# Kernel optimization log

Hardware: AMD Instinct MI355X
Metric: run time of the kernel (lower is better)

The kernel has to match this reference:

```python
import jax, jax.numpy as jnp
import numpy as np

ALPHA = 0.2  # LeakyReLU negative slope


def setup_inputs() -> dict:
    key = jax.random.key(0)
    k1, k2, k3 = jax.random.split(key, 3)
    B, N, F_in, F_out = 8, 2048, 256, 256
    h = jax.random.normal(k1, (B, N, F_in), dtype=jnp.float32)
    adj = jax.random.randint(k2, (B, N, N), 0, 2, dtype=jnp.int32)
    # xavier_uniform for W [F_in, F_out]
    limit = float(np.sqrt(6.0 / (F_in + F_out)))
    W = jax.random.uniform(k3, (F_in, F_out), dtype=jnp.float32, minval=-limit, maxval=limit)
    return {"h": h, "adj": adj, "W": W}


def reference(h, adj, W):
    # h: [B,N,F_in], W: [F_in,F_out] -> Wh: [B,N,F_out]
    Wh = jnp.einsum('bnf,fo->bno', h, W)
    # (Wh_i + Wh_j).sum(-1) == s[p] + s[q] with s = Wh.sum(-1); avoids [B,N,N,F] tensor
    s = Wh.sum(axis=-1)  # [B,N]
    e = jax.nn.leaky_relu(s[:, :, None] + s[:, None, :], negative_slope=ALPHA)  # [B,N,N]
    e = jnp.where(adj == 0, -jnp.inf, e)
    alpha = jax.nn.softmax(e, axis=-1)  # masked softmax over neighbors
    # dropout is identity in eval mode
    h_prime = jnp.einsum('bpq,bqo->bpo', alpha, Wh)  # [B,N,F_out]
    return h_prime
```

## Files before the change

### kernel.cpp

```cpp
#include <hip/hip_runtime.h>
#include <hip/hip_bf16.h>
#include <stdint.h>

#define LEAKY_ALPHA 0.2f

using f32x4 = __attribute__((ext_vector_type(4))) float;
using u32x2 = __attribute__((ext_vector_type(2))) unsigned int;
using u32x4 = __attribute__((ext_vector_type(4))) unsigned int;
using i32x4 = __attribute__((ext_vector_type(4))) int;
using s16x8 = __attribute__((ext_vector_type(8))) short;

static __device__ __forceinline__ unsigned short f2bf(float x) {
  __hip_bfloat16 b = __float2bfloat16(x);
  return __builtin_bit_cast(unsigned short, b);
}

__global__ __launch_bounds__(256) void gat_prep(
    const float* __restrict__ W, __hip_bfloat16* __restrict__ WT,
    float* __restrict__ wsum)
{
  const int o = blockIdx.x;
  const int t = threadIdx.x;
  WT[o * 256 + t] = __float2bfloat16(W[t * 256 + o]);
  float u = W[o * 256 + t];
#pragma unroll
  for (int off = 1; off < 64; off <<= 1) u += __shfl_xor(u, off, 64);
  __shared__ float red[4];
  if ((t & 63) == 0) red[t >> 6] = u;
  __syncthreads();
  if (t == 0) wsum[o] = red[0] + red[1] + red[2] + red[3];
}

__global__ __launch_bounds__(256) void gat_wh2(
    const float* __restrict__ h, const __hip_bfloat16* __restrict__ WT,
    const float* __restrict__ wsum, __hip_bfloat16* __restrict__ WhT,
    float* __restrict__ s)
{
  const int b = blockIdx.x >> 5;
  const int q0 = (blockIdx.x & 31) * 64;
  const int t = threadIdx.x;
  const int wid = t >> 6, lane = t & 63;

  __shared__ __align__(16) unsigned char Bh[64 * 512];
  __shared__ __align__(16) unsigned char Aw[256 * 128];
  __shared__ __align__(16) float wsl[256];

  wsl[t] = wsum[t];
  __syncthreads();

  {
    const int q = t >> 2;
    const int fs = (t & 3) * 64;
    const float* hrow = h + ((size_t)(b * 2048 + q0 + q)) * 256 + fs;
    float sp = 0.f;
#pragma unroll
    for (int c = 0; c < 8; ++c) {
      const f32x4 a  = *(const f32x4*)&hrow[c * 8];
      const f32x4 bq = *(const f32x4*)&hrow[c * 8 + 4];
      const f32x4 wa = *(const f32x4*)&wsl[fs + c * 8];
      const f32x4 wb = *(const f32x4*)&wsl[fs + c * 8 + 4];
      sp += a[0]*wa[0] + a[1]*wa[1] + a[2]*wa[2] + a[3]*wa[3]
          + bq[0]*wb[0] + bq[1]*wb[1] + bq[2]*wb[2] + bq[3]*wb[3];
      u32x4 pk;
      pk[0] = (unsigned)f2bf(a[0])  | ((unsigned)f2bf(a[1])  << 16);
      pk[1] = (unsigned)f2bf(a[2])  | ((unsigned)f2bf(a[3])  << 16);
      pk[2] = (unsigned)f2bf(bq[0]) | ((unsigned)f2bf(bq[1]) << 16);
      pk[3] = (unsigned)f2bf(bq[2]) | ((unsigned)f2bf(bq[3]) << 16);
      const int boff = q * 512 + ((fs * 2 + c * 16) ^ ((q & 7) << 4));
      *(u32x4*)&Bh[boff] = pk;
    }
    sp += __shfl_xor(sp, 1, 64);
    sp += __shfl_xor(sp, 2, 64);
    if ((t & 3) == 0) s[b * 2048 + q0 + q] = sp;
  }

  f32x4 acc[4][4];
#pragma unroll
  for (int i = 0; i < 4; ++i)
#pragma unroll
    for (int j = 0; j < 4; ++j) acc[i][j] = (f32x4)(0.f);

  for (int it = 0; it < 4; ++it) {
    const int f0 = it * 64;
    __syncthreads();
#pragma unroll
    for (int j = 0; j < 8; ++j) {
      const int o = (t >> 3) + 32 * j;
      const int c = t & 7;
      const u32x4 v = *(const u32x4*)&WT[o * 256 + f0 + c * 8];
      *(u32x4*)&Aw[o * 128 + ((c * 16) ^ ((o & 7) << 4))] = v;
    }
    __syncthreads();
#pragma unroll
    for (int kt = 0; kt < 2; ++kt) {
      const int kb = kt * 64 + ((lane >> 4) << 4);
      s16x8 af[4], bf[4];
#pragma unroll
      for (int qt = 0; qt < 4; ++qt) {
        const int qr = qt * 16 + (lane & 15);
        af[qt] = *(const s16x8*)&Bh[qr * 512 + ((f0 * 2 + kb) ^ ((qr & 7) << 4))];
      }
#pragma unroll
      for (int ot = 0; ot < 4; ++ot) {
        const int orow = wid * 64 + ot * 16 + (lane & 15);
        bf[ot] = *(const s16x8*)&Aw[orow * 128 + (kb ^ ((orow & 7) << 4))];
      }
#pragma unroll
      for (int qt = 0; qt < 4; ++qt)
#pragma unroll
        for (int ot = 0; ot < 4; ++ot)
          acc[qt][ot] = __builtin_amdgcn_mfma_f32_16x16x32_bf16(
              af[qt], bf[ot], acc[qt][ot], 0, 0, 0);
    }
  }

  __hip_bfloat16* __restrict__ WhTb = WhT + (size_t)b * 256 * 2048;
#pragma unroll
  for (int qt = 0; qt < 4; ++qt)
#pragma unroll
    for (int ot = 0; ot < 4; ++ot) {
      const int o = wid * 64 + ot * 16 + (lane & 15);
      const int ql = q0 + qt * 16 + ((lane >> 4) << 2);
      u32x2 pk;
      pk[0] = (unsigned)f2bf(acc[qt][ot][0]) | ((unsigned)f2bf(acc[qt][ot][1]) << 16);
      pk[1] = (unsigned)f2bf(acc[qt][ot][2]) | ((unsigned)f2bf(acc[qt][ot][3]) << 16);
      *(u32x2*)&WhTb[(size_t)o * 2048 + ql] = pk;
    }
}

__global__ __launch_bounds__(512, 4) void gat_attn(
    const int* __restrict__ adj, const float* __restrict__ s,
    const __hip_bfloat16* __restrict__ WhT, float* __restrict__ out)
{
  const int N = 2048;
  const int bid = blockIdx.x;
  const int swz = (bid & 7) * 64 + (bid >> 3);
  const int b = swz >> 6;
  const int p0 = (swz & 63) * 32;
  const int t = threadIdx.x;
  const int wid = t >> 6, lane = t & 63;

  __shared__ __align__(16) unsigned char Bs[2][256 * 128];
  __shared__ __align__(16) unsigned char Wt[2][32 * 128];
  __shared__ __align__(16) float red_sh[8];
  __shared__ __align__(16) float l_sh[32];

  const int ep = t >> 4;
  const int eq4 = (t & 15) * 4;
  const int* __restrict__ adjrow = adj + ((size_t)(b * N + p0 + ep)) * N;
  const float* __restrict__ sB = s + b * N;
  const __hip_bfloat16* __restrict__ WhTb = WhT + (size_t)b * 256 * 2048;

  const int so = t >> 3;
  const int q16 = t & 7;

  i32x4 av = *(const i32x4*)&adjrow[eq4];
  f32x4 sv = *(const f32x4*)&sB[eq4];
  u32x4 breg[4];
#pragma unroll
  for (int j = 0; j < 4; ++j)
    breg[j] = *(const u32x4*)&WhTb[(size_t)(so + 64 * j) * 2048 + q16 * 8];

  const f32x4 s4 = *(const f32x4*)&sB[t * 4];
  float bm = fmaxf(fmaxf(s4[0], s4[1]), fmaxf(s4[2], s4[3]));
#pragma unroll
  for (int off = 1; off < 64; off <<= 1) bm = fmaxf(bm, __shfl_xor(bm, off, 64));
  if (lane == 0) red_sh[wid] = bm;
  const float s_p = sB[p0 + ep];
  __syncthreads();
  float smax = red_sh[0];
#pragma unroll
  for (int k = 1; k < 8; ++k) smax = fmaxf(smax, red_sh[k]);
  const float xm = s_p + smax;
  const float m_p = (xm > 0.f) ? xm : (LEAKY_ALPHA * xm);

  f32x4 acc[2][2];
#pragma unroll
  for (int pt = 0; pt < 2; ++pt)
#pragma unroll
    for (int ot = 0; ot < 2; ++ot) acc[pt][ot] = (f32x4)(0.f);
  float lacc = 0.f;

#define GAT_TILE(BI, QQ)                                                      \
  do {                                                                        \
    float wv[4];                                                              \
    _Pragma("unroll")                                                         \
    for (int i = 0; i < 4; ++i) {                                             \
      const float x = s_p + sv[i];                                            \
      const float le = (x > 0.f) ? x : (LEAKY_ALPHA * x);                     \
      const float w = __expf(le - m_p);                                       \
      wv[i] = (av[i] != 0) ? w : 0.f;                                         \
      lacc += wv[i];                                                          \
    }                                                                         \
    {                                                                         \
      u32x2 pw;                                                               \
      pw[0] = (unsigned)f2bf(wv[0]) | ((unsigned)f2bf(wv[1]) << 16);          \
      pw[1] = (unsigned)f2bf(wv[2]) | ((unsigned)f2bf(wv[3]) << 16);          \
      *(u32x2*)&Wt[BI][ep * 128 + ((eq4 * 2) ^ ((ep & 7) << 4))] = pw;        \
    }                                                                         \
    _Pragma("unroll")                                                         \
    for (int j = 0; j < 4; ++j) {                                             \
      const int o = so + 64 * j;                                              \
      *(u32x4*)&Bs[BI][o * 128 + ((q16 * 16) ^ ((o & 7) << 4))] = breg[j];    \
    }                                                                         \
    if ((QQ) + 64 < N) {                                                      \
      av = *(const i32x4*)&adjrow[(QQ) + 64 + eq4];                           \
      sv = *(const f32x4*)&sB[(QQ) + 64 + eq4];                               \
      _Pragma("unroll")                                                       \
      for (int j = 0; j < 4; ++j)                                             \
        breg[j] = *(const u32x4*)&WhTb[(size_t)(so + 64 * j) * 2048 +         \
                                       (QQ) + 64 + q16 * 8];                  \
    }                                                                         \
    asm volatile("s_waitcnt lgkmcnt(0)" ::: "memory");                        \
    __builtin_amdgcn_s_barrier();                                             \
    asm volatile("" ::: "memory");                                            \
    {                                                                         \
      s16x8 afr[2][2], bfr[2][2];                                             \
      _Pragma("unroll")                                                       \
      for (int pt = 0; pt < 2; ++pt)                                          \
        _Pragma("unroll")                                                     \
        for (int kt = 0; kt < 2; ++kt) {                                      \
          const int pa = pt * 16 + (lane & 15);                               \
          const int kb = kt * 64 + ((lane >> 4) << 4);                        \
          afr[pt][kt] =                                                       \
              *(const s16x8*)&Wt[BI][pa * 128 + (kb ^ ((pa & 7) << 4))];      \
        }                                                                     \
      _Pragma("unroll")                                                       \
      for (int ot = 0; ot < 2; ++ot)                                          \
        _Pragma("unroll")                                                     \
        for (int kt = 0; kt < 2; ++kt) {                                      \
          const int ob = wid * 32 + ot * 16 + (lane & 15);                    \
          const int kb = kt * 64 + ((lane >> 4) << 4);                        \
          bfr[ot][kt] =                                                       \
              *(const s16x8*)&Bs[BI][ob * 128 + (kb ^ ((ob & 7) << 4))];      \
        }                                                                     \
      _Pragma("unroll")                                                       \
      for (int pt = 0; pt < 2; ++pt)                                          \
        _Pragma("unroll")                                                     \
        for (int ot = 0; ot < 2; ++ot)                                        \
          _Pragma("unroll")                                                   \
          for (int kt = 0; kt < 2; ++kt)                                      \
            acc[pt][ot] = __builtin_amdgcn_mfma_f32_16x16x32_bf16(            \
                afr[pt][kt], bfr[ot][kt], acc[pt][ot], 0, 0, 0);              \
    }                                                                         \
  } while (0)

  for (int q0 = 0; q0 < N; q0 += 128) {
    GAT_TILE(0, q0);
    GAT_TILE(1, q0 + 64);
  }
#undef GAT_TILE

  lacc += __shfl_xor(lacc, 1, 64);
  lacc += __shfl_xor(lacc, 2, 64);
  lacc += __shfl_xor(lacc, 4, 64);
  lacc += __shfl_xor(lacc, 8, 64);
  if ((t & 15) == 0) l_sh[ep] = lacc;
  __syncthreads();

#pragma unroll
  for (int pt = 0; pt < 2; ++pt) {
    const f32x4 lv = *(const f32x4*)&l_sh[pt * 16 + ((lane >> 4) << 2)];
    f32x4 inv;
#pragma unroll
    for (int r = 0; r < 4; ++r) inv[r] = 1.f / lv[r];
#pragma unroll
    for (int ot = 0; ot < 2; ++ot) {
      const int o = wid * 32 + ot * 16 + (lane & 15);
#pragma unroll
      for (int r = 0; r < 4; ++r) {
        const int row = p0 + pt * 16 + ((lane >> 4) << 2) + r;
        out[((size_t)(b * N + row)) * 256 + o] = acc[pt][ot][r] * inv[r];
      }
    }
  }
}

extern "C" void kernel_launch(void* const* d_in, const int* in_sizes, int n_in,
                              void* d_out, int out_size, void* d_ws, size_t ws_size,
                              hipStream_t stream) {
  const float* h = (const float*)d_in[0];
  const int* adj = (const int*)d_in[1];
  const float* W = (const float*)d_in[2];
  float* out = (float*)d_out;

  char* ws = (char*)d_ws;
  __hip_bfloat16* WhT = (__hip_bfloat16*)ws;
  float* s = (float*)(ws + (size_t)8 * 1024 * 1024);
  __hip_bfloat16* WT = (__hip_bfloat16*)(ws + (size_t)8 * 1024 * 1024 + 65536);
  float* wsum = (float*)(ws + (size_t)8 * 1024 * 1024 + 65536 + 131072);

  gat_prep<<<256, 256, 0, stream>>>(W, WT, wsum);
  gat_wh2<<<256, 256, 0, stream>>>(h, WT, wsum, WhT, s);
  gat_attn<<<512, 512, 0, stream>>>(adj, s, WhT, out);
}
```

Measured before the change: 57.23 us.

## Load WhT B-fragments directly into registers, widen k-tile to 128, drop LDS staging

The attention kernel no longer stages the bf16 WhT tile through shared memory. Each wave loads its MFMA B operands straight from global memory into double-buffered register structs, and the k-tile per iteration grows from 64 to 128 columns. The change also uses a 16-way XOR swizzle for the weight tile and raises wave priority around the MFMA block. It aims to remove LDS write and read traffic and cut barriers in half. In exchange it needs more VGPRs, which may hurt occupancy under launch_bounds(512,4), and the direct global loads are less coalesced.

```diff
diff --git a/kernel.cpp b/kernel.cpp
--- a/kernel.cpp
+++ b/kernel.cpp
@@ -128,6 +128,12 @@
     }
 }
 
+struct GatTile {
+  i32x4 a0, a1;
+  f32x4 s0, s1;
+  u32x4 bv[8];
+};
+
 __global__ __launch_bounds__(512, 4) void gat_attn(
     const int* __restrict__ adj, const float* __restrict__ s,
     const __hip_bfloat16* __restrict__ WhT, float* __restrict__ out)
@@ -140,26 +146,18 @@
   const int t = threadIdx.x;
   const int wid = t >> 6, lane = t & 63;
 
-  __shared__ __align__(16) unsigned char Bs[2][256 * 128];
-  __shared__ __align__(16) unsigned char Wt[2][32 * 128];
+  __shared__ __align__(16) unsigned char Wt[2][32 * 256];
   __shared__ __align__(16) float red_sh[8];
   __shared__ __align__(16) float l_sh[32];
 
   const int ep = t >> 4;
-  const int eq4 = (t & 15) * 4;
+  const int eq = (t & 15) * 8;
   const int* __restrict__ adjrow = adj + ((size_t)(b * N + p0 + ep)) * N;
   const float* __restrict__ sB = s + b * N;
   const __hip_bfloat16* __restrict__ WhTb = WhT + (size_t)b * 256 * 2048;
-
-  const int so = t >> 3;
-  const int q16 = t & 7;
-
-  i32x4 av = *(const i32x4*)&adjrow[eq4];
-  f32x4 sv = *(const f32x4*)&sB[eq4];
-  u32x4 breg[4];
-#pragma unroll
-  for (int j = 0; j < 4; ++j)
-    breg[j] = *(const u32x4*)&WhTb[(size_t)(so + 64 * j) * 2048 + q16 * 8];
+  const __hip_bfloat16* __restrict__ bbase =
+      WhTb + (size_t)(wid * 32 + (lane & 15)) * 2048 + ((lane >> 4) << 3);
+  const int wchunk = (t & 15) ^ (ep & 15);
 
   const f32x4 s4 = *(const f32x4*)&sB[t * 4];
   float bm = fmaxf(fmaxf(s4[0], s4[1]), fmaxf(s4[2], s4[3]));
@@ -181,73 +179,87 @@
     for (int ot = 0; ot < 2; ++ot) acc[pt][ot] = (f32x4)(0.f);
   float lacc = 0.f;
 
-#define GAT_TILE(BI, QQ)                                                      \
+  GatTile TA, TB;
+  TA.a0 = *(const i32x4*)&adjrow[eq];
+  TA.a1 = *(const i32x4*)&adjrow[eq + 4];
+  TA.s0 = *(const f32x4*)&sB[eq];
+  TA.s1 = *(const f32x4*)&sB[eq + 4];
+#pragma unroll
+  for (int ot = 0; ot < 2; ++ot)
+#pragma unroll
+    for (int kt = 0; kt < 4; ++kt)
+      TA.bv[ot * 4 + kt] = *(const u32x4*)&bbase[ot * 16 * 2048 + kt * 32];
+
+#define GAT_TILE(BI, QQ, CUR, NXT)                                            \
   do {                                                                        \
-    float wv[4];                                                              \
+                                                  \
+    float wv[8];                                                              \
+    const float sq[8] = {CUR.s0[0], CUR.s0[1], CUR.s0[2], CUR.s0[3],          \
+                         CUR.s1[0], CUR.s1[1], CUR.s1[2], CUR.s1[3]};         \
+    const int avm[8] = {CUR.a0[0], CUR.a0[1], CUR.a0[2], CUR.a0[3],           \
+                        CUR.a1[0], CUR.a1[1], CUR.a1[2], CUR.a1[3]};          \
     _Pragma("unroll")                                                         \
-    for (int i = 0; i < 4; ++i) {                                             \
-      const float x = s_p + sv[i];                                            \
+    for (int i = 0; i < 8; ++i) {                                             \
+      const float x = s_p + sq[i];                                            \
       const float le = (x > 0.f) ? x : (LEAKY_ALPHA * x);                     \
       const float w = __expf(le - m_p);                                       \
-      wv[i] = (av[i] != 0) ? w : 0.f;                                         \
+      wv[i] = (avm[i] != 0) ? w : 0.f;                                        \
       lacc += wv[i];                                                          \
     }                                                                         \
     {                                                                         \
-      u32x2 pw;                                                               \
-      pw[0] = (unsigned)f2bf(wv[0]) | ((unsigned)f2bf(wv[1]) << 16);          \
-      pw[1] = (unsigned)f2bf(wv[2]) | ((unsigned)f2bf(wv[3]) << 16);          \
-      *(u32x2*)&Wt[BI][ep * 128 + ((eq4 * 2) ^ ((ep & 7) << 4))] = pw;        \
-    }                                                                         \
-    _Pragma("unroll")                                                         \
-    for (int j = 0; j < 4; ++j) {                                             \
-      const int o = so + 64 * j;                                              \
-      *(u32x4*)&Bs[BI][o * 128 + ((q16 * 16) ^ ((o & 7) << 4))] = breg[j];    \
-    }                                                                         \
-    if ((QQ) + 64 < N) {                                                      \
-      av = *(const i32x4*)&adjrow[(QQ) + 64 + eq4];                           \
-      sv = *(const f32x4*)&sB[(QQ) + 64 + eq4];                               \
+      u32x4 pw;                                                               \
       _Pragma("unroll")                                                       \
-      for (int j = 0; j < 4; ++j)                                             \
-        breg[j] = *(const u32x4*)&WhTb[(size_t)(so + 64 * j) * 2048 +         \
-                                       (QQ) + 64 + q16 * 8];                  \
+      for (int k2 = 0; k2 < 4; ++k2)                                          \
+        pw[k2] = (unsigned)f2bf(wv[2 * k2]) |                                 \
+                 ((unsigned)f2bf(wv[2 * k2 + 1]) << 16);                      \
+      *(u32x4*)&Wt[BI][ep * 256 + wchunk * 16] = pw;                          \
+    }                                                                         \
+                                              \
+    if ((QQ) + 128 < N) {                                                     \
+      NXT.a0 = *(const i32x4*)&adjrow[(QQ) + 128 + eq];                       \
+      NXT.a1 = *(const i32x4*)&adjrow[(QQ) + 128 + eq + 4];                   \
+      NXT.s0 = *(const f32x4*)&sB[(QQ) + 128 + eq];                           \
+      NXT.s1 = *(const f32x4*)&sB[(QQ) + 128 + eq + 4];                       \
     }                                                                         \
     asm volatile("s_waitcnt lgkmcnt(0)" ::: "memory");                        \
     __builtin_amdgcn_s_barrier();                                             \
     asm volatile("" ::: "memory");                                            \
     {                                                                         \
-      s16x8 afr[2][2], bfr[2][2];                                             \
+      s16x8 afr[2][4];                                                        \
       _Pragma("unroll")                                                       \
       for (int pt = 0; pt < 2; ++pt)                                          \
         _Pragma("unroll")                                                     \
-        for (int kt = 0; kt < 2; ++kt) {                                      \
+        for (int kt = 0; kt < 4; ++kt) {                                      \
           const int pa = pt * 16 + (lane & 15);                               \
-          const int kb = kt * 64 + ((lane >> 4) << 4);                        \
-          afr[pt][kt] =                                                       \
-              *(const s16x8*)&Wt[BI][pa * 128 + (kb ^ ((pa & 7) << 4))];      \
+          const int ck = (kt * 4 + (lane >> 4)) ^ (pa & 15);                  \
+          afr[pt][kt] = *(const s16x8*)&Wt[BI][pa * 256 + ck * 16];           \
         }                                                                     \
-      _Pragma("unroll")                                                       \
-      for (int ot = 0; ot < 2; ++ot)                                          \
-        _Pragma("unroll")                                                     \
-        for (int kt = 0; kt < 2; ++kt) {                                      \
-          const int ob = wid * 32 + ot * 16 + (lane & 15);                    \
-          const int kb = kt * 64 + ((lane >> 4) << 4);                        \
-          bfr[ot][kt] =                                                       \
-              *(const s16x8*)&Bs[BI][ob * 128 + (kb ^ ((ob & 7) << 4))];      \
-        }                                                                     \
+      __builtin_amdgcn_s_setprio(1);                                          \
       _Pragma("unroll")                                                       \
       for (int pt = 0; pt < 2; ++pt)                                          \
         _Pragma("unroll")                                                     \
         for (int ot = 0; ot < 2; ++ot)                                        \
           _Pragma("unroll")                                                   \
-          for (int kt = 0; kt < 2; ++kt)                                      \
+          for (int kt = 0; kt < 4; ++kt)                                      \
             acc[pt][ot] = __builtin_amdgcn_mfma_f32_16x16x32_bf16(            \
-                afr[pt][kt], bfr[ot][kt], acc[pt][ot], 0, 0, 0);              \
+                afr[pt][kt], __builtin_bit_cast(s16x8, CUR.bv[ot * 4 + kt]),  \
+                acc[pt][ot], 0, 0, 0);                                        \
+      __builtin_amdgcn_s_setprio(0);                                          \
+    }                                                                         \
+           \
+    if ((QQ) + 128 < N) {                                                     \
+      _Pragma("unroll")                                                       \
+      for (int ot = 0; ot < 2; ++ot)                                          \
+        _Pragma("unroll")                                                     \
+        for (int kt = 0; kt < 4; ++kt)                                        \
+          NXT.bv[ot * 4 + kt] =                                               \
+              *(const u32x4*)&bbase[ot * 16 * 2048 + (QQ) + 128 + kt * 32];   \
     }                                                                         \
   } while (0)
 
-  for (int q0 = 0; q0 < N; q0 += 128) {
-    GAT_TILE(0, q0);
-    GAT_TILE(1, q0 + 64);
+  for (int q0 = 0; q0 < N; q0 += 256) {
+    GAT_TILE(0, q0, TA, TB);
+    GAT_TILE(1, q0 + 128, TB, TA);
   }
 #undef GAT_TILE
 
```

Result: slower. 119.7 us (+109.2%).

## Restructure attention kernel to register-only MFMA with no shared memory

Applied to the files above, without the earlier changes.

The attention kernel now gives each block 16 query rows and 256 threads. Each wave computes softmax weights directly in registers in MFMA operand layout and feeds WhT fragments loaded straight from global memory. This removes the LDS staging buffers and per-tile barriers, and uses exp2 with a max-of-two-FMAs form of LeakyReLU. The cost is that each block re-reads the WhT tile from global or L2 with half the row reuse, and every block recomputes the row max over s.

```diff
diff --git a/kernel.cpp b/kernel.cpp
--- a/kernel.cpp
+++ b/kernel.cpp
@@ -128,152 +128,125 @@
     }
 }
 
-__global__ __launch_bounds__(512, 4) void gat_attn(
+__global__ __launch_bounds__(256, 4) void gat_attn(
     const int* __restrict__ adj, const float* __restrict__ s,
     const __hip_bfloat16* __restrict__ WhT, float* __restrict__ out)
 {
   const int N = 2048;
   const int bid = blockIdx.x;
-  const int swz = (bid & 7) * 64 + (bid >> 3);
-  const int b = swz >> 6;
-  const int p0 = (swz & 63) * 32;
+  const int swz = (bid & 7) * 128 + (bid >> 3);
+  const int b = swz >> 7;
+  const int p0 = (swz & 127) * 16;
   const int t = threadIdx.x;
   const int wid = t >> 6, lane = t & 63;
-
-  __shared__ __align__(16) unsigned char Bs[2][256 * 128];
-  __shared__ __align__(16) unsigned char Wt[2][32 * 128];
-  __shared__ __align__(16) float red_sh[8];
-  __shared__ __align__(16) float l_sh[32];
-
-  const int ep = t >> 4;
-  const int eq4 = (t & 15) * 4;
-  const int* __restrict__ adjrow = adj + ((size_t)(b * N + p0 + ep)) * N;
+  const int lp = lane & 15;
+  const int lq = (lane >> 4) << 3;
+
+  const int* __restrict__ adjp = adj + (size_t)(b * N + p0 + lp) * N + lq;
   const float* __restrict__ sB = s + b * N;
-  const __hip_bfloat16* __restrict__ WhTb = WhT + (size_t)b * 256 * 2048;
-
-  const int so = t >> 3;
-  const int q16 = t & 7;
-
-  i32x4 av = *(const i32x4*)&adjrow[eq4];
-  f32x4 sv = *(const f32x4*)&sB[eq4];
-  u32x4 breg[4];
-#pragma unroll
-  for (int j = 0; j < 4; ++j)
-    breg[j] = *(const u32x4*)&WhTb[(size_t)(so + 64 * j) * 2048 + q16 * 8];
-
-  const f32x4 s4 = *(const f32x4*)&sB[t * 4];
-  float bm = fmaxf(fmaxf(s4[0], s4[1]), fmaxf(s4[2], s4[3]));
+  const float* __restrict__ sq = sB + lq;
+  const __hip_bfloat16* __restrict__ Ab =
+      WhT + (size_t)b * 256 * 2048 + (size_t)(wid * 64 + lp) * 2048 + lq;
+
+  float bm = -1e30f;
+#pragma unroll
+  for (int i = 0; i < 8; ++i) {
+    const f32x4 v = *(const f32x4*)&sB[(i * 64 + lane) * 4];
+    bm = fmaxf(bm, fmaxf(fmaxf(v[0], v[1]), fmaxf(v[2], v[3])));
+  }
 #pragma unroll
   for (int off = 1; off < 64; off <<= 1) bm = fmaxf(bm, __shfl_xor(bm, off, 64));
-  if (lane == 0) red_sh[wid] = bm;
-  const float s_p = sB[p0 + ep];
-  __syncthreads();
-  float smax = red_sh[0];
-#pragma unroll
-  for (int k = 1; k < 8; ++k) smax = fmaxf(smax, red_sh[k]);
-  const float xm = s_p + smax;
+  const float s_p = sB[p0 + lp];
+  const float xm = s_p + bm;
   const float m_p = (xm > 0.f) ? xm : (LEAKY_ALPHA * xm);
-
-  f32x4 acc[2][2];
-#pragma unroll
-  for (int pt = 0; pt < 2; ++pt)
-#pragma unroll
-    for (int ot = 0; ot < 2; ++ot) acc[pt][ot] = (f32x4)(0.f);
+  const float L2E  = 1.4426950408889634f;
+  const float L2EA = L2E * LEAKY_ALPHA;
+  const float c1 = (s_p - m_p) * L2E;
+  const float c2 = (LEAKY_ALPHA * s_p - m_p) * L2E;
+
+  f32x4 acc0 = (f32x4)(0.f), acc1 = (f32x4)(0.f);
+  f32x4 acc2 = (f32x4)(0.f), acc3 = (f32x4)(0.f);
   float lacc = 0.f;
 
-#define GAT_TILE(BI, QQ)                                                      \
+  i32x4 aE0, aE1, aO0, aO1;
+  f32x4 sE0, sE1, sO0, sO1;
+  u32x4 fE0, fE1, fE2, fE3, fO0, fO1, fO2, fO3;
+
+  aE0 = *(const i32x4*)&adjp[0];   aE1 = *(const i32x4*)&adjp[4];
+  sE0 = *(const f32x4*)&sq[0];     sE1 = *(const f32x4*)&sq[4];
+  fE0 = *(const u32x4*)&Ab[0];
+  fE1 = *(const u32x4*)&Ab[16 * 2048];
+  fE2 = *(const u32x4*)&Ab[32 * 2048];
+  fE3 = *(const u32x4*)&Ab[48 * 2048];
+  aO0 = *(const i32x4*)&adjp[32];  aO1 = *(const i32x4*)&adjp[36];
+  sO0 = *(const f32x4*)&sq[32];    sO1 = *(const f32x4*)&sq[36];
+  fO0 = *(const u32x4*)&Ab[32];
+  fO1 = *(const u32x4*)&Ab[16 * 2048 + 32];
+  fO2 = *(const u32x4*)&Ab[32 * 2048 + 32];
+  fO3 = *(const u32x4*)&Ab[48 * 2048 + 32];
+
+#define GAT_TILE(A0, A1, S0, S1, F0, F1, F2, F3, QQ)                          \
   do {                                                                        \
-    float wv[4];                                                              \
-    _Pragma("unroll")                                                         \
-    for (int i = 0; i < 4; ++i) {                                             \
-      const float x = s_p + sv[i];                                            \
-      const float le = (x > 0.f) ? x : (LEAKY_ALPHA * x);                     \
-      const float w = __expf(le - m_p);                                       \
-      wv[i] = (av[i] != 0) ? w : 0.f;                                         \
-      lacc += wv[i];                                                          \
+    float wv[8];                                                              \
+    _Pragma("unroll")                                                         \
+    for (int j = 0; j < 4; ++j) {                                             \
+      const float t1 = __builtin_fmaf(S0[j], L2E, c1);                        \
+      const float t2 = __builtin_fmaf(S0[j], L2EA, c2);                       \
+      const float w = exp2f(fmaxf(t1, t2));                                   \
+      wv[j] = (A0[j] != 0) ? w : 0.f;                                         \
     }                                                                         \
-    {                                                                         \
-      u32x2 pw;                                                               \
-      pw[0] = (unsigned)f2bf(wv[0]) | ((unsigned)f2bf(wv[1]) << 16);          \
-      pw[1] = (unsigned)f2bf(wv[2]) | ((unsigned)f2bf(wv[3]) << 16);          \
-      *(u32x2*)&Wt[BI][ep * 128 + ((eq4 * 2) ^ ((ep & 7) << 4))] = pw;        \
+    _Pragma("unroll")                                                         \
+    for (int j = 0; j < 4; ++j) {                                             \
+      const float t1 = __builtin_fmaf(S1[j], L2E, c1);                        \
+      const float t2 = __builtin_fmaf(S1[j], L2EA, c2);                       \
+      const float w = exp2f(fmaxf(t1, t2));                                   \
+      wv[4 + j] = (A1[j] != 0) ? w : 0.f;                                     \
     }                                                                         \
     _Pragma("unroll")                                                         \
-    for (int j = 0; j < 4; ++j) {                                             \
-      const int o = so + 64 * j;                                              \
-      *(u32x4*)&Bs[BI][o * 128 + ((q16 * 16) ^ ((o & 7) << 4))] = breg[j];    \
-    }                                                                         \
+    for (int j = 0; j < 8; ++j) lacc += wv[j];                                \
+    u32x4 pw;                                                                 \
+    _Pragma("unroll")                                                         \
+    for (int k2 = 0; k2 < 4; ++k2)                                            \
+      pw[k2] = (unsigned)f2bf(wv[2 * k2]) |                                   \
+               ((unsigned)f2bf(wv[2 * k2 + 1]) << 16);                        \
+    const s16x8 bfr = __builtin_bit_cast(s16x8, pw);                          \
+    acc0 = __builtin_amdgcn_mfma_f32_16x16x32_bf16(                           \
+        __builtin_bit_cast(s16x8, F0), bfr, acc0, 0, 0, 0);                   \
+    acc1 = __builtin_amdgcn_mfma_f32_16x16x32_bf16(                           \
+        __builtin_bit_cast(s16x8, F1), bfr, acc1, 0, 0, 0);                   \
+    acc2 = __builtin_amdgcn_mfma_f32_16x16x32_bf16(                           \
+        __builtin_bit_cast(s16x8, F2), bfr, acc2, 0, 0, 0);                   \
+    acc3 = __builtin_amdgcn_mfma_f32_16x16x32_bf16(                           \
+        __builtin_bit_cast(s16x8, F3), bfr, acc3, 0, 0, 0);                   \
     if ((QQ) + 64 < N) {                                                      \
-      av = *(const i32x4*)&adjrow[(QQ) + 64 + eq4];                           \
-      sv = *(const f32x4*)&sB[(QQ) + 64 + eq4];                               \
-      _Pragma("unroll")                                                       \
-      for (int j = 0; j < 4; ++j)                                             \
-        breg[j] = *(const u32x4*)&WhTb[(size_t)(so + 64 * j) * 2048 +         \
-                                       (QQ) + 64 + q16 * 8];                  \
-    }                                                                         \
-    asm volatile("s_waitcnt lgkmcnt(0)" ::: "memory");                        \
-    __builtin_amdgcn_s_barrier();                                             \
-    asm volatile("" ::: "memory");                                            \
-    {                                                                         \
-      s16x8 afr[2][2], bfr[2][2];                                             \
-      _Pragma("unroll")                                                       \
-      for (int pt = 0; pt < 2; ++pt)                                          \
-        _Pragma("unroll")                                                     \
-        for (int kt = 0; kt < 2; ++kt) {                                      \
-          const int pa = pt * 16 + (lane & 15);                               \
-          const int kb = kt * 64 + ((lane >> 4) << 4);                        \
-          afr[pt][kt] =                                                       \
-              *(const s16x8*)&Wt[BI][pa * 128 + (kb ^ ((pa & 7) << 4))];      \
-        }                                                                     \
-      _Pragma("unroll")                                                       \
-      for (int ot = 0; ot < 2; ++ot)                                          \
-        _Pragma("unroll")                                                     \
-        for (int kt = 0; kt < 2; ++kt) {                                      \
-          const int ob = wid * 32 + ot * 16 + (lane & 15);                    \
-          const int kb = kt * 64 + ((lane >> 4) << 4);                        \
-          bfr[ot][kt] =                                                       \
-              *(const s16x8*)&Bs[BI][ob * 128 + (kb ^ ((ob & 7) << 4))];      \
-        }                                                                     \
-      _Pragma("unroll")                                                       \
-      for (int pt = 0; pt < 2; ++pt)                                          \
-        _Pragma("unroll")                                                     \
-        for (int ot = 0; ot < 2; ++ot)                                        \
-          _Pragma("unroll")                                                   \
-          for (int kt = 0; kt < 2; ++kt)                                      \
-            acc[pt][ot] = __builtin_amdgcn_mfma_f32_16x16x32_bf16(            \
-                afr[pt][kt], bfr[ot][kt], acc[pt][ot], 0, 0, 0);              \
+      A0 = *(const i32x4*)&adjp[(QQ) + 64];                                   \
+      A1 = *(const i32x4*)&adjp[(QQ) + 68];                                   \
+      S0 = *(const f32x4*)&sq[(QQ) + 64];                                     \
+      S1 = *(const f32x4*)&sq[(QQ) + 68];                                     \
+      F0 = *(const u32x4*)&Ab[(QQ) + 64];                                     \
+      F1 = *(const u32x4*)&Ab[16 * 2048 + (QQ) + 64];                         \
+      F2 = *(const u32x4*)&Ab[32 * 2048 + (QQ) + 64];                         \
+      F3 = *(const u32x4*)&Ab[48 * 2048 + (QQ) + 64];                         \
     }                                                                         \
   } while (0)
 
-  for (int q0 = 0; q0 < N; q0 += 128) {
-    GAT_TILE(0, q0);
-    GAT_TILE(1, q0 + 64);
+  for (int q0 = 0; q0 < N; q0 += 64) {
+    GAT_TILE(aE0, aE1, sE0, sE1, fE0, fE1, fE2, fE3, q0);
+    GAT_TILE(aO0, aO1, sO0, sO1, fO0, fO1, fO2, fO3, q0 + 32);
   }
 #undef GAT_TILE
 
-  lacc += __shfl_xor(lacc, 1, 64);
-  lacc += __shfl_xor(lacc, 2, 64);
-  lacc += __shfl_xor(lacc, 4, 64);
-  lacc += __shfl_xor(lacc, 8, 64);
-  if ((t & 15) == 0) l_sh[ep] = lacc;
-  __syncthreads();
-
-#pragma unroll
-  for (int pt = 0; pt < 2; ++pt) {
-    const f32x4 lv = *(const f32x4*)&l_sh[pt * 16 + ((lane >> 4) << 2)];
-    f32x4 inv;
-#pragma unroll
-    for (int r = 0; r < 4; ++r) inv[r] = 1.f / lv[r];
-#pragma unroll
-    for (int ot = 0; ot < 2; ++ot) {
-      const int o = wid * 32 + ot * 16 + (lane & 15);
-#pragma unroll
-      for (int r = 0; r < 4; ++r) {
-        const int row = p0 + pt * 16 + ((lane >> 4) << 2) + r;
-        out[((size_t)(b * N + row)) * 256 + o] = acc[pt][ot][r] * inv[r];
-      }
-    }
-  }
+  lacc += __shfl_xor(lacc, 16, 64);
+  lacc += __shfl_xor(lacc, 32, 64);
+  const float inv = 1.f / lacc;
+
+  float* __restrict__ orow = out + (size_t)(b * N + p0 + lp) * 256;
+  const int ob = wid * 64 + ((lane >> 4) << 2);
+  acc0 *= inv; acc1 *= inv; acc2 *= inv; acc3 *= inv;
+  *(f32x4*)&orow[ob]      = acc0;
+  *(f32x4*)&orow[ob + 16] = acc1;
+  *(f32x4*)&orow[ob + 32] = acc2;
+  *(f32x4*)&orow[ob + 48] = acc3;
 }
 
 extern "C" void kernel_launch(void* const* d_in, const int* in_sizes, int n_in,
@@ -292,5 +265,5 @@
 
   gat_prep<<<256, 256, 0, stream>>>(W, WT, wsum);
   gat_wh2<<<256, 256, 0, stream>>>(h, WT, wsum, WhT, s);
-  gat_attn<<<512, 512, 0, stream>>>(adj, s, WhT, out);
-}
+  gat_attn<<<1024, 256, 0, stream>>>(adj, s, WhT, out);
+}
```

Measured after the change: 206.1 us. +260.1%, slower.
